# Kernel tuning notes

Measured on AMD Instinct MI355X. Metric: run time of the kernel, lower is better.

Reference implementation:

```python
import jax, jax.numpy as jnp
import numpy as np

N, C, K = 100000, 128, 27
EPS = 1e-5


def sparse_conv(x, W, idx_in, idx_out):
    """Gather-GEMM-scatter sparse conv: sum_k scatter_add(idx_out[k], x[idx_in[k]] @ W[k]).
    x: [N, Cin], W: [K, Cin, Cout], idx_in/idx_out: [K, M] int32."""
    n = x.shape[0]
    out0 = jnp.zeros((n, W.shape[2]), x.dtype)

    def body(acc, inp):
        w, ii, io = inp
        contrib = jnp.take(x, ii, axis=0) @ w  # [M, Cout]
        return acc.at[io].add(contrib), None

    out, _ = jax.lax.scan(body, out0, (W, idx_in, idx_out))
    return out


def batch_norm(x, gamma, beta):
    # BatchNorm1d training-mode forward: per-channel batch stats over N
    mu = jnp.mean(x, axis=0)
    var = jnp.var(x, axis=0)
    return (x - mu) * jax.lax.rsqrt(var + EPS) * gamma + beta


def setup_inputs() -> dict:
    key = jax.random.key(0)
    ks = jax.random.split(key, 5)
    w_scale = 1.0 / np.sqrt(K * C)
    x = jax.random.normal(ks[0], (N, C), dtype=jnp.float32)
    W1 = jax.random.normal(ks[1], (K, C, C), dtype=jnp.float32) * w_scale
    W2 = jax.random.normal(ks[2], (K, C, C), dtype=jnp.float32) * w_scale
    g1 = jnp.ones((C,), jnp.float32)
    b1 = jnp.zeros((C,), jnp.float32)
    g2 = jnp.ones((C,), jnp.float32)
    b2 = jnp.zeros((C,), jnp.float32)
    idx_in = jax.random.randint(ks[3], (K, N), 0, N, dtype=jnp.int32)
    idx_out = jax.random.randint(ks[4], (K, N), 0, N, dtype=jnp.int32)
    return {"x": x, "W1": W1, "g1": g1, "b1": b1, "W2": W2, "g2": g2,
            "b2": b2, "idx_in": idx_in, "idx_out": idx_out}


def reference(x, W1, g1, b1, W2, g2, b2, idx_in, idx_out):
    # net: conv -> BN -> ReLU -> conv -> BN
    h = sparse_conv(x, W1, idx_in, idx_out)
    h = jax.nn.relu(batch_norm(h, g1, b1))
    h = sparse_conv(h, W2, idx_in, idx_out)
    h = batch_norm(h, g2, b2)
    # downsample = Identity (inc == outc, stride == 1); residual add + ReLU
    return jax.nn.relu(h + x)
```

## Files before the change

### kernel.cpp

```cpp
#include <hip/hip_runtime.h>

typedef __attribute__((ext_vector_type(8))) short bf16x8;
typedef __attribute__((ext_vector_type(4))) float f32x4;
typedef __attribute__((ext_vector_type(4))) unsigned short u16x4;
typedef __attribute__((ext_vector_type(4))) unsigned u32x4;

#define CH 4096
#define MAXNT 4096

__device__ __forceinline__ unsigned short f2b(float f) {
    unsigned u = __builtin_bit_cast(unsigned, f);
    u += 0x7fffu + ((u >> 16) & 1u);
    return (unsigned short)(u >> 16);
}

__global__ void zero_f32(float* __restrict__ p, long total) {
    long i = ((long)blockIdx.x * blockDim.x + threadIdx.x) * 4;
    if (i + 3 < total) {
        *(f32x4*)(p + i) = (f32x4){0.f, 0.f, 0.f, 0.f};
    } else {
        for (long t = i; t < total; ++t) p[t] = 0.f;
    }
}

__global__ void cvt_bf16(const float* __restrict__ x, unsigned short* __restrict__ o, long total) {
    long i = ((long)blockIdx.x * blockDim.x + threadIdx.x) * 4;
    if (i >= total) return;
    f32x4 v = *(const f32x4*)(x + i);
    u16x4 r;
#pragma unroll
    for (int t = 0; t < 4; ++t) r[t] = f2b(v[t]);
    *(u16x4*)(o + i) = r;
}

__global__ void prep_w(const float* __restrict__ W1, const float* __restrict__ W2,
                       unsigned short* __restrict__ Wb1, unsigned short* __restrict__ Wb2,
                       int kelems) {
    int tid = blockIdx.x * 256 + threadIdx.x;
    if (tid >= 2 * kelems) return;
    int which = (tid >= kelems) ? 1 : 0;
    int rem = which ? (tid - kelems) : tid;
    int k = rem >> 14;
    int r2 = rem & 16383;
    int f = r2 >> 9;
    int lane = (r2 >> 3) & 63;
    int j = r2 & 7;
    int kk = f >> 3, c = f & 7;
    int cin = kk * 32 + (lane >> 4) * 8 + j;
    int cout = c * 16 + (lane & 15);
    const float* W = which ? W2 : W1;
    unsigned short* Wb = which ? Wb2 : Wb1;
    Wb[rem] = f2b(W[(size_t)k * 16384 + cin * 128 + cout]);
}


__global__ void pass_hist32(const int* __restrict__ io, int* __restrict__ cnt,
                            int n, int NT, int NCH) {
    __shared__ int hist[MAXNT];
    const int k = blockIdx.x / NCH, c = blockIdx.x % NCH;
    for (int i = threadIdx.x; i < NT; i += 256) hist[i] = 0;
    __syncthreads();
    const int m1 = min(n, (c + 1) * CH);
    const int* p = io + (size_t)k * n;
    for (int m = c * CH + threadIdx.x; m < m1; m += 256)
        atomicAdd(&hist[((unsigned)p[m]) >> 5], 1);
    __syncthreads();
    for (int rt = threadIdx.x; rt < NT; rt += 256)
        cnt[(size_t)(k * NT + rt) * NCH + c] = hist[rt];
}

__global__ void scan_part(const int* __restrict__ cnt, int* __restrict__ bsum, int nbins) {
    __shared__ int ls[256];
    int base = blockIdx.x * 4096 + threadIdx.x * 16;
    int s = 0;
#pragma unroll
    for (int i = 0; i < 16; ++i) { int idx = base + i; if (idx < nbins) s += cnt[idx]; }
    ls[threadIdx.x] = s; __syncthreads();
    for (int o = 128; o > 0; o >>= 1) {
        if ((int)threadIdx.x < o) ls[threadIdx.x] += ls[threadIdx.x + o];
        __syncthreads();
    }
    if (threadIdx.x == 0) bsum[blockIdx.x] = ls[0];
}

__global__ void scan_bsum(int* __restrict__ bsum, int nb, int* __restrict__ sptr, int nbins) {
    if (threadIdx.x == 0 && blockIdx.x == 0) {
        int run = 0;
        for (int i = 0; i < nb; ++i) { int t = bsum[i]; bsum[i] = run; run += t; }
        sptr[nbins] = run;
    }
}

__global__ void scan_final(const int* __restrict__ cnt, const int* __restrict__ bsum,
                           int* __restrict__ sptr, int nbins) {
    __shared__ int ls[256];
    const int tid = threadIdx.x;
    int base = blockIdx.x * 4096 + tid * 16;
    int loc[16];
    int s = 0;
#pragma unroll
    for (int i = 0; i < 16; ++i) {
        int idx = base + i;
        int v = (idx < nbins) ? cnt[idx] : 0;
        loc[i] = s; s += v;
    }
    ls[tid] = s; __syncthreads();
    for (int o = 1; o < 256; o <<= 1) {
        int add = (tid >= o) ? ls[tid - o] : 0;
        __syncthreads();
        ls[tid] += add;
        __syncthreads();
    }
    int excl = ls[tid] - s + bsum[blockIdx.x];
#pragma unroll
    for (int i = 0; i < 16; ++i) {
        int idx = base + i;
        if (idx < nbins) sptr[idx] = excl + loc[i];
    }
}

__global__ void pass_scatter32(const int* __restrict__ io, const int* __restrict__ iin,
                               const int* __restrict__ sptr, unsigned* __restrict__ pay,
                               int n, int NT, int NCH) {
    __shared__ int base[MAXNT];
    const int k = blockIdx.x / NCH, c = blockIdx.x % NCH;
    for (int rt = threadIdx.x; rt < NT; rt += 256)
        base[rt] = sptr[(size_t)(k * NT + rt) * NCH + c];
    __syncthreads();
    const int m1 = min(n, (c + 1) * CH);
    const int* pio = io + (size_t)k * n;
    const int* pii = iin + (size_t)k * n;
    for (int m = c * CH + threadIdx.x; m < m1; m += 256) {
        int r = pio[m];
        int ii = pii[m];
        int p = atomicAdd(&base[r >> 5], 1);
        pay[p] = ((unsigned)ii << 5) | (unsigned)(r & 31);
    }
}

__global__ __launch_bounds__(256) void conv_ms(
    const unsigned short* __restrict__ xin,
    const unsigned short* __restrict__ Wb,
    const unsigned* __restrict__ pay,
    const int* __restrict__ sptr,
    float* __restrict__ h,
    int n, int NT, int NCH, int K)
{
    const int lane = threadIdx.x & 63;
    const int wv = threadIdx.x >> 6;
    const int kg = lane >> 4, l15 = lane & 15;
    const int rt = blockIdx.x * 4 + wv;
    if (rt >= NT) return;
    const int sA = ((kg & 1) << 5) + l15;
    const int sB = sA + 16;
    const bool lo = (kg < 2);

    f32x4 acc[2][8];
#pragma unroll
    for (int o = 0; o < 2; ++o)
#pragma unroll
        for (int c = 0; c < 8; ++c) acc[o][c] = (f32x4){0.f, 0.f, 0.f, 0.f};

    for (int k = 0; k < K; ++k) {
        const unsigned short* wk = Wb + (size_t)k * 16384 + (size_t)lane * 8;
        const int e0 = sptr[(size_t)(k * NT + rt) * NCH];
        const int e1 = sptr[(size_t)(k * NT + rt + 1) * NCH];
        unsigned pv = (e0 + l15 < e1) ? pay[e0 + l15] : 0xFFFFFFFFu;

        for (int e = e0; e < e1; e += 16) {
            unsigned pvn = (e + 16 + l15 < e1) ? pay[e + 16 + l15] : 0xFFFFFFFFu;
            int ii = (pv != 0xFFFFFFFFu) ? (int)(pv >> 5) : 0;
            const unsigned short* xr = xin + (size_t)ii * 128 + kg * 8;

            bf16x8 oh0, oh1;
#pragma unroll
            for (int j = 0; j < 8; ++j) {
                int q = kg * 8 + j;
                unsigned pq = (unsigned)__shfl((int)pv, q & 15, 64);
                int rl = (q < 16 && pq != 0xFFFFFFFFu) ? (int)(pq & 31u) : 999;
                oh0[j] = (short)((rl == l15) ? 0x3F80 : 0);
                oh1[j] = (short)((rl == 16 + l15) ? 0x3F80 : 0);
            }

#pragma unroll
            for (int hh = 0; hh < 2; ++hh) {
                f32x4 y[4];
#pragma unroll
                for (int c4 = 0; c4 < 4; ++c4) y[c4] = (f32x4){0.f, 0.f, 0.f, 0.f};
#pragma unroll
                for (int kk = 0; kk < 4; ++kk) {
                    bf16x8 a = *(const bf16x8*)(xr + kk * 32);
#pragma unroll
                    for (int c4 = 0; c4 < 4; ++c4) {
                        bf16x8 b = *(const bf16x8*)(wk + (size_t)(kk * 8 + hh * 4 + c4) * 512);
                        y[c4] = __builtin_amdgcn_mfma_f32_16x16x32_bf16(a, b, y[c4], 0, 0, 0);
                    }
                }
                unsigned cv0[4], cv1[4];
#pragma unroll
                for (int c4 = 0; c4 < 4; ++c4) {
                    asm("v_cvt_pk_bf16_f32 %0, %1, %2" : "=v"(cv0[c4]) : "v"(y[c4][0]), "v"(y[c4][1]));
                    asm("v_cvt_pk_bf16_f32 %0, %1, %2" : "=v"(cv1[c4]) : "v"(y[c4][2]), "v"(y[c4][3]));
                }
#pragma unroll
                for (int c4 = 0; c4 < 4; ++c4) {
                    unsigned v0 = (unsigned)__shfl((int)cv0[c4], sA, 64);
                    unsigned v1 = (unsigned)__shfl((int)cv1[c4], sA, 64);
                    unsigned v2 = (unsigned)__shfl((int)cv0[c4], sB, 64);
                    unsigned v3 = (unsigned)__shfl((int)cv1[c4], sB, 64);
                    u32x4 t = (u32x4){lo ? v0 : 0u, lo ? v1 : 0u, lo ? v2 : 0u, lo ? v3 : 0u};
                    bf16x8 bb = __builtin_bit_cast(bf16x8, t);
                    acc[0][hh * 4 + c4] = __builtin_amdgcn_mfma_f32_16x16x32_bf16(oh0, bb, acc[0][hh * 4 + c4], 0, 0, 0);
                    acc[1][hh * 4 + c4] = __builtin_amdgcn_mfma_f32_16x16x32_bf16(oh1, bb, acc[1][hh * 4 + c4], 0, 0, 0);
                }
            }
            pv = pvn;
        }
    }

    const int r0 = rt * 32;
#pragma unroll
    for (int o = 0; o < 2; ++o)
#pragma unroll
        for (int c = 0; c < 8; ++c)
#pragma unroll
            for (int j = 0; j < 4; ++j) {
                int r = r0 + o * 16 + kg * 4 + j;
                if (r < n) h[(size_t)r * 128 + l15 + 16 * c] = acc[o][c][j];
            }
}

__global__ __launch_bounds__(512) void conv_atomic(
    const unsigned short* __restrict__ xin, const unsigned short* __restrict__ Wb,
    const int* __restrict__ idx_in, const int* __restrict__ idx_out,
    float* __restrict__ out, int n) {
    __shared__ unsigned short wlds[16384];
    const int k = blockIdx.y;
    const int m0 = blockIdx.x * 256;
    {
        const bf16x8* src = (const bf16x8*)(Wb + (size_t)k * 16384);
        bf16x8* dst = (bf16x8*)wlds;
        for (int i = threadIdx.x; i < 2048; i += 512) dst[i] = src[i];
    }
    __syncthreads();
    const int wave = threadIdx.x >> 6;
    const int lane = threadIdx.x & 63;
    const int kg = lane >> 4;
    const int l15 = lane & 15;
    const int* iin  = idx_in  + (size_t)k * n;
    const int* iout = idx_out + (size_t)k * n;
    const int mbase = m0 + wave * 32;
    int arow0, arow1;
    { int m = mbase + l15;      arow0 = (m < n) ? iin[m] : 0; }
    { int m = mbase + 16 + l15; arow1 = (m < n) ? iin[m] : 0; }
    f32x4 acc[2][8];
#pragma unroll
    for (int s = 0; s < 2; ++s)
#pragma unroll
        for (int c = 0; c < 8; ++c) acc[s][c] = (f32x4){0.f, 0.f, 0.f, 0.f};
#pragma unroll
    for (int kk = 0; kk < 4; ++kk) {
        bf16x8 a0 = *(const bf16x8*)(xin + (size_t)arow0 * 128 + kk * 32 + kg * 8);
        bf16x8 a1 = *(const bf16x8*)(xin + (size_t)arow1 * 128 + kk * 32 + kg * 8);
#pragma unroll
        for (int c = 0; c < 8; ++c) {
            bf16x8 b = *(const bf16x8*)(wlds + ((kk * 8 + c) * 64 + lane) * 8);
            acc[0][c] = __builtin_amdgcn_mfma_f32_16x16x32_bf16(a0, b, acc[0][c], 0, 0, 0);
            acc[1][c] = __builtin_amdgcn_mfma_f32_16x16x32_bf16(a1, b, acc[1][c], 0, 0, 0);
        }
    }
#pragma unroll
    for (int s = 0; s < 2; ++s)
#pragma unroll
        for (int j = 0; j < 4; ++j) {
            int m = mbase + s * 16 + kg * 4 + j;
            if (m < n) {
                long orow = iout[m];
                float* dst = out + orow * 128 + l15;
#pragma unroll
                for (int c = 0; c < 8; ++c) atomicAdd(dst + c * 16, acc[s][c][j]);
            }
        }
}


__global__ void bn_stats(const float* __restrict__ h, float* __restrict__ stats, int n) {
    const int c = threadIdx.x & 127;
    const int half = threadIdx.x >> 7;
    const int r0 = blockIdx.x * 256;
    const int rend = min(r0 + 256, n);
    float s = 0.f, s2 = 0.f;
    for (int r = r0 + half; r < rend; r += 2) {
        float v = h[(size_t)r * 128 + c];
        s += v; s2 += v * v;
    }
    __shared__ float ls[256], ls2[256];
    ls[threadIdx.x] = s; ls2[threadIdx.x] = s2;
    __syncthreads();
    if (half == 0) {
        atomicAdd(&stats[c], ls[c] + ls[128 + c]);
        atomicAdd(&stats[128 + c], ls2[c] + ls2[128 + c]);
    }
}

__global__ void bn_finalize(float* stats, const float* __restrict__ g,
                            const float* __restrict__ b, float inv_n) {
    int c = threadIdx.x;
    float mu = stats[c] * inv_n;
    float var = fmaxf(stats[128 + c] * inv_n - mu * mu, 0.f);
    float sc = g[c] * rsqrtf(var + 1e-5f);
    stats[256 + c] = sc;
    stats[384 + c] = b[c] - mu * sc;
}

__global__ void bn_relu_bf16(const float* __restrict__ h, const float* __restrict__ stats,
                             unsigned short* __restrict__ hb, long total) {
    long i = ((long)blockIdx.x * 256 + threadIdx.x) * 4;
    if (i >= total) return;
    int c = (int)(i & 127);
    f32x4 v = *(const f32x4*)(h + i);
    u16x4 r;
#pragma unroll
    for (int t = 0; t < 4; ++t) {
        float y = fmaxf(v[t] * stats[256 + c + t] + stats[384 + c + t], 0.f);
        r[t] = f2b(y);
    }
    *(u16x4*)(hb + i) = r;
}

__global__ void bn_res_relu(float* __restrict__ out, const float* __restrict__ stats,
                            const float* __restrict__ x, long total) {
    long i = ((long)blockIdx.x * 256 + threadIdx.x) * 4;
    if (i >= total) return;
    int c = (int)(i & 127);
    f32x4 h = *(const f32x4*)(out + i);
    f32x4 xv = *(const f32x4*)(x + i);
    f32x4 r;
#pragma unroll
    for (int t = 0; t < 4; ++t)
        r[t] = fmaxf(h[t] * stats[256 + c + t] + stats[384 + c + t] + xv[t], 0.f);
    *(f32x4*)(out + i) = r;
}

extern "C" void kernel_launch(void* const* d_in, const int* in_sizes, int n_in,
                              void* d_out, int out_size, void* d_ws, size_t ws_size,
                              hipStream_t stream) {
    const float* x  = (const float*)d_in[0];
    const float* W1 = (const float*)d_in[1];
    const float* g1 = (const float*)d_in[2];
    const float* b1 = (const float*)d_in[3];
    const float* W2 = (const float*)d_in[4];
    const float* g2 = (const float*)d_in[5];
    const float* b2 = (const float*)d_in[6];
    const int* idx_in  = (const int*)d_in[7];
    const int* idx_out = (const int*)d_in[8];

    const int n = in_sizes[0] / 128;
    const int K = in_sizes[1] / 16384;
    const long total = (long)n * 128;
    const int nk = K * n;
    float* acc = (float*)d_out;

    char* ws = (char*)d_ws;
    auto align256 = [](size_t v) { return (v + 255) & ~255ULL; };

    const int NT  = (n + 31) / 32;
    const int NCH = (n + CH - 1) / CH;
    const long nbinsS = (long)K * NT * NCH;
    const long nbS = (nbinsS + 4095) / 4096;

    size_t off = 0;
    const size_t o_slabA = off; off = align256(off + (size_t)total * 2);
    const size_t o_Wb1   = off; off = align256(off + (size_t)K * 16384 * 2);
    const size_t o_Wb2   = off; off = align256(off + (size_t)K * 16384 * 2);
    const size_t o_stats = off; off = align256(off + 1024 * 4);
    const size_t o_pay   = off; off = align256(off + (size_t)nk * 4);
    const size_t o_cnt   = off; off = align256(off + (size_t)nbinsS * 4);
    const size_t o_sptr  = off; off = align256(off + ((size_t)nbinsS + 1) * 4);
    const size_t o_bsum  = off; off = align256(off + ((size_t)nbS + 2) * 4);
    const bool fast_ok = (NT <= MAXNT) && (off <= ws_size);

    unsigned short* slabA = (unsigned short*)(ws + o_slabA);
    unsigned short* Wb1   = (unsigned short*)(ws + o_Wb1);
    unsigned short* Wb2   = (unsigned short*)(ws + o_Wb2);
    float* stats          = (float*)(ws + o_stats);
    unsigned* pay         = (unsigned*)(ws + o_pay);
    int* cnt              = (int*)(ws + o_cnt);
    int* sptr             = (int*)(ws + o_sptr);
    int* bsum             = (int*)(ws + o_bsum);

    const dim3 b256(256);
    const int gCvt = (int)((total / 4 + 255) / 256);
    const int kelems = K * 16384;

    hipLaunchKernelGGL(zero_f32, dim3(1), b256, 0, stream, stats, (long)1024);
    hipLaunchKernelGGL(cvt_bf16, dim3(gCvt), b256, 0, stream, x, slabA, total);
    hipLaunchKernelGGL(prep_w, dim3((2 * kelems + 255) / 256), b256, 0, stream,
                       W1, W2, Wb1, Wb2, kelems);

    if (fast_ok) {
        const int gSort = K * NCH;
        hipLaunchKernelGGL(pass_hist32, dim3(gSort), b256, 0, stream, idx_out, cnt, n, NT, NCH);
        hipLaunchKernelGGL(scan_part, dim3((int)nbS), b256, 0, stream, cnt, bsum, (int)nbinsS);
        hipLaunchKernelGGL(scan_bsum, dim3(1), dim3(64), 0, stream, bsum, (int)nbS, sptr, (int)nbinsS);
        hipLaunchKernelGGL(scan_final, dim3((int)nbS), b256, 0, stream, cnt, bsum, sptr, (int)nbinsS);
        hipLaunchKernelGGL(pass_scatter32, dim3(gSort), b256, 0, stream,
                           idx_out, idx_in, sptr, pay, n, NT, NCH);

        const int gConv = (NT + 3) / 4;
        for (int conv = 0; conv < 2; ++conv) {
            const unsigned short* Wb = conv ? Wb2 : Wb1;
            float* st = stats + conv * 512;
            hipLaunchKernelGGL(conv_ms, dim3(gConv), b256, 0, stream,
                               slabA, Wb, pay, sptr, acc, n, NT, NCH, K);
            hipLaunchKernelGGL(bn_stats, dim3((n + 255) / 256), b256, 0, stream, acc, st, n);
            hipLaunchKernelGGL(bn_finalize, dim3(1), dim3(128), 0, stream, st,
                               conv ? g2 : g1, conv ? b2 : b1, 1.0f / n);
            if (conv == 0)
                hipLaunchKernelGGL(bn_relu_bf16, dim3(gCvt), b256, 0, stream, acc, st, slabA, total);
            else
                hipLaunchKernelGGL(bn_res_relu, dim3(gCvt), b256, 0, stream, acc, st, x, total);
        }
    } else {
        for (int conv = 0; conv < 2; ++conv) {
            const unsigned short* Wb = conv ? Wb2 : Wb1;
            float* st = stats + conv * 512;
            hipLaunchKernelGGL(zero_f32, dim3(gCvt), b256, 0, stream, acc, total);
            hipLaunchKernelGGL(conv_atomic, dim3((n + 255) / 256, K), dim3(512), 0, stream,
                               slabA, Wb, idx_in, idx_out, acc, n);
            hipLaunchKernelGGL(bn_stats, dim3((n + 255) / 256), b256, 0, stream, acc, st, n);
            hipLaunchKernelGGL(bn_finalize, dim3(1), dim3(128), 0, stream, st,
                               conv ? g2 : g1, conv ? b2 : b1, 1.0f / n);
            if (conv == 0)
                hipLaunchKernelGGL(bn_relu_bf16, dim3(gCvt), b256, 0, stream, acc, st, slabA, total);
            else
                hipLaunchKernelGGL(bn_res_relu, dim3(gCvt), b256, 0, stream, acc, st, x, total);
        }
    }
}
```

Before: 999.1 us.

## Split conv kernel offsets across two grid halves and pack two 16-entry groups per one-hot MFMA

The gather-GEMM conv kernel now splits the K kernel offsets across a second grid dimension. Each half writes its own fp32 partial buffer, and a new merge kernel adds the two while computing batch-norm statistics. Inside the loop, each step now processes 32 pair entries. Two 16-row gather GEMMs fill both halves of the one-hot scatter MFMA operand, where previously half of it was zero. This doubles grid parallelism and halves the wasted MFMA work, at the cost of an extra fp32 buffer and extra read/write traffic in the merge pass.

```diff
diff --git a/kernel.cpp b/kernel.cpp
--- a/kernel.cpp
+++ b/kernel.cpp
@@ -143,17 +143,22 @@
     const unsigned short* __restrict__ Wb,
     const unsigned* __restrict__ pay,
     const int* __restrict__ sptr,
-    float* __restrict__ h,
-    int n, int NT, int NCH, int K)
+    float* __restrict__ h0, float* __restrict__ h1,
+    int n, int NT, int NCH, int K, int KH)
 {
     const int lane = threadIdx.x & 63;
     const int wv = threadIdx.x >> 6;
     const int kg = lane >> 4, l15 = lane & 15;
     const int rt = blockIdx.x * 4 + wv;
     if (rt >= NT) return;
+    const int kh = blockIdx.y;
+    const int k0 = kh * KH, k1 = min(K, k0 + KH);
+    float* __restrict__ hout = kh ? h1 : h0;
+
     const int sA = ((kg & 1) << 5) + l15;
     const int sB = sA + 16;
     const bool lo = (kg < 2);
+    const int ohBase = ((kg & 1) << 3) | (lo ? 0 : 32);
 
     f32x4 acc[2][8];
 #pragma unroll
@@ -161,23 +166,26 @@
 #pragma unroll
         for (int c = 0; c < 8; ++c) acc[o][c] = (f32x4){0.f, 0.f, 0.f, 0.f};
 
-    for (int k = 0; k < K; ++k) {
+    for (int k = k0; k < k1; ++k) {
         const unsigned short* wk = Wb + (size_t)k * 16384 + (size_t)lane * 8;
         const int e0 = sptr[(size_t)(k * NT + rt) * NCH];
         const int e1 = sptr[(size_t)(k * NT + rt + 1) * NCH];
-        unsigned pv = (e0 + l15 < e1) ? pay[e0 + l15] : 0xFFFFFFFFu;
-
-        for (int e = e0; e < e1; e += 16) {
-            unsigned pvn = (e + 16 + l15 < e1) ? pay[e + 16 + l15] : 0xFFFFFFFFu;
-            int ii = (pv != 0xFFFFFFFFu) ? (int)(pv >> 5) : 0;
-            const unsigned short* xr = xin + (size_t)ii * 128 + kg * 8;
-
+
+        for (int e = e0; e < e1; e += 32) {
+            unsigned pvA = (e + l15 < e1) ? pay[e + l15] : 0xFFFFFFFFu;
+            unsigned pvB = (e + 16 + l15 < e1) ? pay[e + 16 + l15] : 0xFFFFFFFFu;
+            const bool hasB = (e + 16 < e1);
+            int iiA = (pvA != 0xFFFFFFFFu) ? (int)(pvA >> 5) : 0;
+            int iiB = (pvB != 0xFFFFFFFFu) ? (int)(pvB >> 5) : 0;
+            const unsigned short* xrA = xin + (size_t)iiA * 128 + kg * 8;
+            const unsigned short* xrB = xin + (size_t)iiB * 128 + kg * 8;
+
+            unsigned pvME = lo ? pvA : pvB;
             bf16x8 oh0, oh1;
 #pragma unroll
             for (int j = 0; j < 8; ++j) {
-                int q = kg * 8 + j;
-                unsigned pq = (unsigned)__shfl((int)pv, q & 15, 64);
-                int rl = (q < 16 && pq != 0xFFFFFFFFu) ? (int)(pq & 31u) : 999;
+                unsigned pq = (unsigned)__shfl((int)pvME, ohBase + j, 64);
+                int rl = (pq != 0xFFFFFFFFu) ? (int)(pq & 31u) : 999;
                 oh0[j] = (short)((rl == l15) ? 0x3F80 : 0);
                 oh1[j] = (short)((rl == 16 + l15) ? 0x3F80 : 0);
             }
@@ -185,36 +193,62 @@
 #pragma unroll
             for (int hh = 0; hh < 2; ++hh) {
                 f32x4 y[4];
+                unsigned cvA0[4], cvA1[4], cvB0[4], cvB1[4];
 #pragma unroll
                 for (int c4 = 0; c4 < 4; ++c4) y[c4] = (f32x4){0.f, 0.f, 0.f, 0.f};
 #pragma unroll
                 for (int kk = 0; kk < 4; ++kk) {
-                    bf16x8 a = *(const bf16x8*)(xr + kk * 32);
+                    bf16x8 a = *(const bf16x8*)(xrA + kk * 32);
 #pragma unroll
                     for (int c4 = 0; c4 < 4; ++c4) {
                         bf16x8 b = *(const bf16x8*)(wk + (size_t)(kk * 8 + hh * 4 + c4) * 512);
                         y[c4] = __builtin_amdgcn_mfma_f32_16x16x32_bf16(a, b, y[c4], 0, 0, 0);
                     }
                 }
-                unsigned cv0[4], cv1[4];
 #pragma unroll
                 for (int c4 = 0; c4 < 4; ++c4) {
-                    asm("v_cvt_pk_bf16_f32 %0, %1, %2" : "=v"(cv0[c4]) : "v"(y[c4][0]), "v"(y[c4][1]));
-                    asm("v_cvt_pk_bf16_f32 %0, %1, %2" : "=v"(cv1[c4]) : "v"(y[c4][2]), "v"(y[c4][3]));
+                    asm("v_cvt_pk_bf16_f32 %0, %1, %2" : "=v"(cvA0[c4]) : "v"(y[c4][0]), "v"(y[c4][1]));
+                    asm("v_cvt_pk_bf16_f32 %0, %1, %2" : "=v"(cvA1[c4]) : "v"(y[c4][2]), "v"(y[c4][3]));
                 }
+                if (hasB) {
+#pragma unroll
+                    for (int c4 = 0; c4 < 4; ++c4) y[c4] = (f32x4){0.f, 0.f, 0.f, 0.f};
+#pragma unroll
+                    for (int kk = 0; kk < 4; ++kk) {
+                        bf16x8 a = *(const bf16x8*)(xrB + kk * 32);
+#pragma unroll
+                        for (int c4 = 0; c4 < 4; ++c4) {
+                            bf16x8 b = *(const bf16x8*)(wk + (size_t)(kk * 8 + hh * 4 + c4) * 512);
+                            y[c4] = __builtin_amdgcn_mfma_f32_16x16x32_bf16(a, b, y[c4], 0, 0, 0);
+                        }
+                    }
+#pragma unroll
+                    for (int c4 = 0; c4 < 4; ++c4) {
+                        asm("v_cvt_pk_bf16_f32 %0, %1, %2" : "=v"(cvB0[c4]) : "v"(y[c4][0]), "v"(y[c4][1]));
+                        asm("v_cvt_pk_bf16_f32 %0, %1, %2" : "=v"(cvB1[c4]) : "v"(y[c4][2]), "v"(y[c4][3]));
+                    }
+                } else {
+#pragma unroll
+                    for (int c4 = 0; c4 < 4; ++c4) { cvB0[c4] = 0; cvB1[c4] = 0; }
+                }
 #pragma unroll
                 for (int c4 = 0; c4 < 4; ++c4) {
-                    unsigned v0 = (unsigned)__shfl((int)cv0[c4], sA, 64);
-                    unsigned v1 = (unsigned)__shfl((int)cv1[c4], sA, 64);
-                    unsigned v2 = (unsigned)__shfl((int)cv0[c4], sB, 64);
-                    unsigned v3 = (unsigned)__shfl((int)cv1[c4], sB, 64);
-                    u32x4 t = (u32x4){lo ? v0 : 0u, lo ? v1 : 0u, lo ? v2 : 0u, lo ? v3 : 0u};
+                    unsigned vA0 = (unsigned)__shfl((int)cvA0[c4], sA, 64);
+                    unsigned vA1 = (unsigned)__shfl((int)cvA1[c4], sA, 64);
+                    unsigned vA2 = (unsigned)__shfl((int)cvA0[c4], sB, 64);
+                    unsigned vA3 = (unsigned)__shfl((int)cvA1[c4], sB, 64);
+                    unsigned vB0 = (unsigned)__shfl((int)cvB0[c4], sA, 64);
+                    unsigned vB1 = (unsigned)__shfl((int)cvB1[c4], sA, 64);
+                    unsigned vB2 = (unsigned)__shfl((int)cvB0[c4], sB, 64);
+                    unsigned vB3 = (unsigned)__shfl((int)cvB1[c4], sB, 64);
+                    u32x4 t = (u32x4){lo ? vA0 : vB0, lo ? vA1 : vB1,
+                                      lo ? vA2 : vB2, lo ? vA3 : vB3};
                     bf16x8 bb = __builtin_bit_cast(bf16x8, t);
-                    acc[0][hh * 4 + c4] = __builtin_amdgcn_mfma_f32_16x16x32_bf16(oh0, bb, acc[0][hh * 4 + c4], 0, 0, 0);
-                    acc[1][hh * 4 + c4] = __builtin_amdgcn_mfma_f32_16x16x32_bf16(oh1, bb, acc[1][hh * 4 + c4], 0, 0, 0);
+                    int ci = hh * 4 + c4;
+                    acc[0][ci] = __builtin_amdgcn_mfma_f32_16x16x32_bf16(oh0, bb, acc[0][ci], 0, 0, 0);
+                    acc[1][ci] = __builtin_amdgcn_mfma_f32_16x16x32_bf16(oh1, bb, acc[1][ci], 0, 0, 0);
                 }
             }
-            pv = pvn;
         }
     }
 
@@ -226,7 +260,7 @@
 #pragma unroll
             for (int j = 0; j < 4; ++j) {
                 int r = r0 + o * 16 + kg * 4 + j;
-                if (r < n) h[(size_t)r * 128 + l15 + 16 * c] = acc[o][c][j];
+                if (r < n) hout[(size_t)r * 128 + l15 + 16 * c] = acc[o][c][j];
             }
 }
 
@@ -303,6 +337,28 @@
     }
 }
 
+__global__ void bn_stats_merge(float* __restrict__ h0, const float* __restrict__ h1,
+                               float* __restrict__ stats, int n) {
+    const int c = threadIdx.x & 127;
+    const int half = threadIdx.x >> 7;
+    const int r0 = blockIdx.x * 256;
+    const int rend = min(r0 + 256, n);
+    float s = 0.f, s2 = 0.f;
+    for (int r = r0 + half; r < rend; r += 2) {
+        size_t idx = (size_t)r * 128 + c;
+        float v = h0[idx] + h1[idx];
+        h0[idx] = v;
+        s += v; s2 += v * v;
+    }
+    __shared__ float ls[256], ls2[256];
+    ls[threadIdx.x] = s; ls2[threadIdx.x] = s2;
+    __syncthreads();
+    if (half == 0) {
+        atomicAdd(&stats[c], ls[c] + ls[128 + c]);
+        atomicAdd(&stats[128 + c], ls2[c] + ls2[128 + c]);
+    }
+}
+
 __global__ void bn_finalize(float* stats, const float* __restrict__ g,
                             const float* __restrict__ b, float inv_n) {
     int c = threadIdx.x;
@@ -374,6 +430,7 @@
     const size_t o_Wb1   = off; off = align256(off + (size_t)K * 16384 * 2);
     const size_t o_Wb2   = off; off = align256(off + (size_t)K * 16384 * 2);
     const size_t o_stats = off; off = align256(off + 1024 * 4);
+    const size_t o_h2    = off; off = align256(off + (size_t)total * 4);
     const size_t o_pay   = off; off = align256(off + (size_t)nk * 4);
     const size_t o_cnt   = off; off = align256(off + (size_t)nbinsS * 4);
     const size_t o_sptr  = off; off = align256(off + ((size_t)nbinsS + 1) * 4);
@@ -384,6 +441,7 @@
     unsigned short* Wb1   = (unsigned short*)(ws + o_Wb1);
     unsigned short* Wb2   = (unsigned short*)(ws + o_Wb2);
     float* stats          = (float*)(ws + o_stats);
+    float* h2             = (float*)(ws + o_h2);
     unsigned* pay         = (unsigned*)(ws + o_pay);
     int* cnt              = (int*)(ws + o_cnt);
     int* sptr             = (int*)(ws + o_sptr);
@@ -408,12 +466,14 @@
                            idx_out, idx_in, sptr, pay, n, NT, NCH);
 
         const int gConv = (NT + 3) / 4;
+        const int KH = (K + 1) / 2;
         for (int conv = 0; conv < 2; ++conv) {
             const unsigned short* Wb = conv ? Wb2 : Wb1;
             float* st = stats + conv * 512;
-            hipLaunchKernelGGL(conv_ms, dim3(gConv), b256, 0, stream,
-                               slabA, Wb, pay, sptr, acc, n, NT, NCH, K);
-            hipLaunchKernelGGL(bn_stats, dim3((n + 255) / 256), b256, 0, stream, acc, st, n);
+            hipLaunchKernelGGL(conv_ms, dim3(gConv, 2), b256, 0, stream,
+                               slabA, Wb, pay, sptr, acc, h2, n, NT, NCH, K, KH);
+            hipLaunchKernelGGL(bn_stats_merge, dim3((n + 255) / 256), b256, 0, stream,
+                               acc, h2, st, n);
             hipLaunchKernelGGL(bn_finalize, dim3(1), dim3(128), 0, stream, st,
                                conv ? g2 : g1, conv ? b2 : b1, 1.0f / n);
             if (conv == 0)
```

Result: slower. 1.489 ms (+49.0%).

## Split conv kernel offsets across two grid halves and merge partials in BN stats

Applied to the files above, without the earlier changes.

The output-stationary conv kernel now launches a 2D grid in which each half processes half of the 27 kernel offsets and writes its own partial output buffer. A new bn_stats_merge kernel adds the two partial buffers, writes the sum back, and accumulates the batch-norm statistics in the same pass. This doubles the number of waves, aiming to fill the GPU better, since the original grid had only about 782 blocks of 4 waves. In exchange it needs an extra 51MB fp32 workspace buffer and adds extra global memory traffic in the merge pass.

```diff
diff --git a/kernel.cpp b/kernel.cpp
--- a/kernel.cpp
+++ b/kernel.cpp
@@ -143,14 +143,18 @@
     const unsigned short* __restrict__ Wb,
     const unsigned* __restrict__ pay,
     const int* __restrict__ sptr,
-    float* __restrict__ h,
-    int n, int NT, int NCH, int K)
+    float* __restrict__ h0, float* __restrict__ h1,
+    int n, int NT, int NCH, int K, int KH)
 {
     const int lane = threadIdx.x & 63;
     const int wv = threadIdx.x >> 6;
     const int kg = lane >> 4, l15 = lane & 15;
     const int rt = blockIdx.x * 4 + wv;
     if (rt >= NT) return;
+    const int kh = blockIdx.y;
+    const int k0 = kh * KH, k1 = min(K, k0 + KH);
+    float* __restrict__ hout = kh ? h1 : h0;
+
     const int sA = ((kg & 1) << 5) + l15;
     const int sB = sA + 16;
     const bool lo = (kg < 2);
@@ -161,7 +165,7 @@
 #pragma unroll
         for (int c = 0; c < 8; ++c) acc[o][c] = (f32x4){0.f, 0.f, 0.f, 0.f};
 
-    for (int k = 0; k < K; ++k) {
+    for (int k = k0; k < k1; ++k) {
         const unsigned short* wk = Wb + (size_t)k * 16384 + (size_t)lane * 8;
         const int e0 = sptr[(size_t)(k * NT + rt) * NCH];
         const int e1 = sptr[(size_t)(k * NT + rt + 1) * NCH];
@@ -210,8 +214,9 @@
                     unsigned v3 = (unsigned)__shfl((int)cv1[c4], sB, 64);
                     u32x4 t = (u32x4){lo ? v0 : 0u, lo ? v1 : 0u, lo ? v2 : 0u, lo ? v3 : 0u};
                     bf16x8 bb = __builtin_bit_cast(bf16x8, t);
-                    acc[0][hh * 4 + c4] = __builtin_amdgcn_mfma_f32_16x16x32_bf16(oh0, bb, acc[0][hh * 4 + c4], 0, 0, 0);
-                    acc[1][hh * 4 + c4] = __builtin_amdgcn_mfma_f32_16x16x32_bf16(oh1, bb, acc[1][hh * 4 + c4], 0, 0, 0);
+                    int ci = hh * 4 + c4;
+                    acc[0][ci] = __builtin_amdgcn_mfma_f32_16x16x32_bf16(oh0, bb, acc[0][ci], 0, 0, 0);
+                    acc[1][ci] = __builtin_amdgcn_mfma_f32_16x16x32_bf16(oh1, bb, acc[1][ci], 0, 0, 0);
                 }
             }
             pv = pvn;
@@ -226,7 +231,7 @@
 #pragma unroll
             for (int j = 0; j < 4; ++j) {
                 int r = r0 + o * 16 + kg * 4 + j;
-                if (r < n) h[(size_t)r * 128 + l15 + 16 * c] = acc[o][c][j];
+                if (r < n) hout[(size_t)r * 128 + l15 + 16 * c] = acc[o][c][j];
             }
 }
 
@@ -292,6 +297,28 @@
     float s = 0.f, s2 = 0.f;
     for (int r = r0 + half; r < rend; r += 2) {
         float v = h[(size_t)r * 128 + c];
+        s += v; s2 += v * v;
+    }
+    __shared__ float ls[256], ls2[256];
+    ls[threadIdx.x] = s; ls2[threadIdx.x] = s2;
+    __syncthreads();
+    if (half == 0) {
+        atomicAdd(&stats[c], ls[c] + ls[128 + c]);
+        atomicAdd(&stats[128 + c], ls2[c] + ls2[128 + c]);
+    }
+}
+
+__global__ void bn_stats_merge(float* __restrict__ h0, const float* __restrict__ h1,
+                               float* __restrict__ stats, int n) {
+    const int c = threadIdx.x & 127;
+    const int half = threadIdx.x >> 7;
+    const int r0 = blockIdx.x * 256;
+    const int rend = min(r0 + 256, n);
+    float s = 0.f, s2 = 0.f;
+    for (int r = r0 + half; r < rend; r += 2) {
+        size_t idx = (size_t)r * 128 + c;
+        float v = h0[idx] + h1[idx];
+        h0[idx] = v;
         s += v; s2 += v * v;
     }
     __shared__ float ls[256], ls2[256];
@@ -374,6 +401,7 @@
     const size_t o_Wb1   = off; off = align256(off + (size_t)K * 16384 * 2);
     const size_t o_Wb2   = off; off = align256(off + (size_t)K * 16384 * 2);
     const size_t o_stats = off; off = align256(off + 1024 * 4);
+    const size_t o_h2    = off; off = align256(off + (size_t)total * 4);
     const size_t o_pay   = off; off = align256(off + (size_t)nk * 4);
     const size_t o_cnt   = off; off = align256(off + (size_t)nbinsS * 4);
     const size_t o_sptr  = off; off = align256(off + ((size_t)nbinsS + 1) * 4);
@@ -384,6 +412,7 @@
     unsigned short* Wb1   = (unsigned short*)(ws + o_Wb1);
     unsigned short* Wb2   = (unsigned short*)(ws + o_Wb2);
     float* stats          = (float*)(ws + o_stats);
+    float* h2             = (float*)(ws + o_h2);
     unsigned* pay         = (unsigned*)(ws + o_pay);
     int* cnt              = (int*)(ws + o_cnt);
     int* sptr             = (int*)(ws + o_sptr);
@@ -408,12 +437,14 @@
                            idx_out, idx_in, sptr, pay, n, NT, NCH);
 
         const int gConv = (NT + 3) / 4;
+        const int KH = (K + 1) / 2;
         for (int conv = 0; conv < 2; ++conv) {
             const unsigned short* Wb = conv ? Wb2 : Wb1;
             float* st = stats + conv * 512;
-            hipLaunchKernelGGL(conv_ms, dim3(gConv), b256, 0, stream,
-                               slabA, Wb, pay, sptr, acc, n, NT, NCH, K);
-            hipLaunchKernelGGL(bn_stats, dim3((n + 255) / 256), b256, 0, stream, acc, st, n);
+            hipLaunchKernelGGL(conv_ms, dim3(gConv, 2), b256, 0, stream,
+                               slabA, Wb, pay, sptr, acc, h2, n, NT, NCH, K, KH);
+            hipLaunchKernelGGL(bn_stats_merge, dim3((n + 255) / 256), b256, 0, stream,
+                               acc, h2, st, n);
             hipLaunchKernelGGL(bn_finalize, dim3(1), dim3(128), 0, stream, st,
                                conv ? g2 : g1, conv ? b2 : b1, 1.0f / n);
             if (conv == 0)
```

New measurement: 985.2 us. Within noise of the previous version (-1.4%).
